# Optimization experiments

Measured on AMD Instinct MI355X. Metric: run time of the kernel, lower is better.

The kernel has to match this reference:

```python
import jax, jax.numpy as jnp
import numpy as np

B, CIN, COUT, T = 64, 2048, 2048, 128
BLOCK = 8            # structured-sparsity block size from _create_structured_sparse_mask
SPARSITY = 0.9       # keep probability per block = 1 - SPARSITY
SPIKE_PROB = 0.1     # binary input spike rate


def setup_inputs() -> dict:
    key = jax.random.key(0)
    k1, k2, k3 = jax.random.split(key, 3)
    # binary input spikes [B, Cin, T] (torch casts to int8; values are 0/1)
    spikes = (jax.random.uniform(k1, (B, CIN, T)) < SPIKE_PROB).astype(jnp.float32)
    # int8 quantized weights held as float32 (values in [-127,127))
    weights = jax.random.randint(k2, (COUT, CIN), -127, 127).astype(jnp.float32)
    # block-structured sparse connectivity mask, block 8x8, keep prob 0.1
    keep = jax.random.uniform(k3, (COUT // BLOCK, CIN // BLOCK)) > SPARSITY
    mask = jnp.repeat(jnp.repeat(keep, BLOCK, axis=0), BLOCK, axis=1).astype(jnp.float32)
    scale_exp = jnp.zeros((COUT,), dtype=jnp.int32)  # weight_scale_exp init zeros
    return {"spikes": spikes, "weights": weights, "mask": mask,
            "scale_exp": scale_exp, "threshold_exp": 7}


def reference(spikes, weights, mask, scale_exp, threshold_exp):
    # spikes: [B, Cin, T]; weights/mask: [Cout, Cin]; scale_exp: [Cout]
    masked_w = weights * mask                              # [Cout, Cin]
    scale = jnp.exp2(scale_exp.astype(jnp.float32))        # 2**weight_scale_exp per channel
    thr = jnp.float32(2.0) ** threshold_exp                # 2**threshold_exp (=128)
    s_t = jnp.transpose(spikes, (2, 0, 1))                 # [T, B, Cin]
    acc0 = jnp.zeros((spikes.shape[0], weights.shape[0]), jnp.float32)

    def step(acc, st):
        # integrate: sparse-masked matmul + power-of-two per-channel scale
        acc = acc + (st @ masked_w.T) * scale              # [B, Cout]
        spk = (acc >= thr).astype(jnp.float32)             # fire
        acc = acc * (1.0 - spk)                            # reset fired neurons to 0
        return acc, spk

    _, out = jax.lax.scan(step, acc0, s_t)                 # out: [T, B, Cout]
    return jnp.transpose(out, (1, 2, 0))                   # [B, Cout, T]
```

## Files before the change

kernel.cpp:

```cpp
#include <hip/hip_runtime.h>
#include <hip/hip_bf16.h>

#define BB   64
#define CIN  2048
#define COUT 2048
#define TT   128

typedef int i32x4 __attribute__((ext_vector_type(4)));

__device__ __forceinline__ void async16(char* lds_dst, const char* g_src) {
    __builtin_amdgcn_global_load_lds(
        (const __attribute__((address_space(1))) void*)g_src,
        (__attribute__((address_space(3))) void*)lds_dst,
        16, 0, 0);
}

__global__ void prep_kernel(const float* __restrict__ spikes,
                            const float* __restrict__ w,
                            const float* __restrict__ msk,
                            char* __restrict__ A,
                            char* __restrict__ Wm) {
    __shared__ float tile[64][33];
    int bid = blockIdx.x;
    int tid = threadIdx.x;

    if (bid < 1024) {
        size_t i = ((size_t)bid * 256 + tid) * 16;
        int out4[4];
#pragma unroll
        for (int q = 0; q < 4; ++q) {
            float4 a = *(const float4*)(w + i + q * 4);
            float4 m = *(const float4*)(msk + i + q * 4);
            int b0 = (int)(char)(int)(a.x * m.x);
            int b1 = (int)(char)(int)(a.y * m.y);
            int b2 = (int)(char)(int)(a.z * m.z);
            int b3 = (int)(char)(int)(a.w * m.w);
            out4[q] = (b0 & 0xFF) | ((b1 & 0xFF) << 8) | ((b2 & 0xFF) << 16) | (b3 << 24);
        }
        *(int4*)(Wm + i) = *(int4*)out4;
        return;
    }

    bid -= 1024;
    int cc = bid & 31;
    int tt = (bid >> 5) & 3;
    int b  = bid >> 7;
    int c0 = cc * 64, t0 = tt * 32;

    int t4 = tid & 7;
    int cr = tid >> 3;
#pragma unroll
    for (int s = 0; s < 2; ++s) {
        int c = cr + s * 32;
        float4 v = *(const float4*)(spikes + ((size_t)b * CIN + c0 + c) * TT + t0 + t4 * 4);
        tile[c][t4 * 4 + 0] = v.x;
        tile[c][t4 * 4 + 1] = v.y;
        tile[c][t4 * 4 + 2] = v.z;
        tile[c][t4 * 4 + 3] = v.w;
    }
    __syncthreads();

    int tw_ = tid >> 4;
    int cq  = tid & 15;
#pragma unroll
    for (int s2 = 0; s2 < 2; ++s2) {
        int tw = tw_ + s2 * 16;
        int packed = 0;
#pragma unroll
        for (int q = 0; q < 4; ++q)
            packed |= ((tile[cq * 4 + q][tw] != 0.f) ? 1 : 0) << (8 * q);
        *(int*)(A + ((size_t)(b * TT) + t0 + tw) * CIN + c0 + cq * 4) = packed;
    }
}

__global__ void __launch_bounds__(256, 4)
snn_gemm_scan(const char* __restrict__ A,
              const char* __restrict__ Wm,
              const int* __restrict__ scale_exp,
              const int* __restrict__ thr_exp,
              float* __restrict__ out) {
    __shared__ __align__(16) union {
        struct { char a[128 * 128]; char b[128 * 128]; } st;
        float c[128 * 68];
    } lds;
    __shared__ unsigned pb[64 * 4];

    const int tid  = threadIdx.x;
    const int lane = tid & 63;
    const int w    = tid >> 6;

    int flat = blockIdx.x;
    int xcd = flat & 7, idx = flat >> 3;
    int b  = xcd * 8 + (idx >> 4);
    int n0 = (idx & 15) * 128;
    int m0 = b * TT;

    int rr = tid >> 3;
    int cg = (tid & 7) ^ (rr & 7);
    const char* gAt = A  + (size_t)(m0 + rr) * CIN + cg * 16;
    const char* gBt = Wm + (size_t)(n0 + rr) * CIN + cg * 16;
    char* sA = (char*)lds.st.a;
    char* sB = (char*)lds.st.b;

    const int wm = (w >> 1) * 64, wn = (w & 1) * 64;
    const int mrow = lane & 15, kc = lane >> 4;
    unsigned offA[4], offB[4];
#pragma unroll
    for (int i = 0; i < 4; ++i) {
        offA[i] = (unsigned)(((wm + i * 16 + mrow) * 8 + (kc ^ (mrow & 7))) * 16);
        offB[i] = (unsigned)(((wn + i * 16 + mrow) * 8 + (kc ^ (mrow & 7))) * 16);
    }

    i32x4 acc[4][4] = {};
    for (int k0 = 0; k0 < CIN; k0 += 128) {
        __syncthreads();
#pragma unroll
        for (int i = 0; i < 4; ++i) {
            async16(sA + (unsigned)(tid + 256 * i) * 16, gAt + k0 + (size_t)(32 * i) * CIN);
            async16(sB + (unsigned)(tid + 256 * i) * 16, gBt + k0 + (size_t)(32 * i) * CIN);
        }
        __syncthreads();

#pragma unroll
        for (int s = 0; s < 2; ++s) {
            const unsigned sx = (unsigned)(s * 64);
            i32x4 av[4], bv[4];
#pragma unroll
            for (int i = 0; i < 4; ++i) av[i] = *(const i32x4*)(sA + (offA[i] ^ sx));
#pragma unroll
            for (int j = 0; j < 4; ++j) bv[j] = *(const i32x4*)(sB + (offB[j] ^ sx));
#pragma unroll
            for (int i = 0; i < 4; ++i)
#pragma unroll
                for (int j = 0; j < 4; ++j)
                    acc[i][j] = __builtin_amdgcn_mfma_i32_16x16x64_i8(
                        av[i], bv[j], acc[i][j], 0, 0, 0);
        }
    }

    const float thr = exp2f((float)thr_exp[0]);

#pragma unroll
    for (int p = 0; p < 2; ++p) {
        __syncthreads();
        if ((w & 1) == p) {
            const int rb = (lane >> 4) * 4;
            const int cb = lane & 15;
#pragma unroll
            for (int i = 0; i < 4; ++i)
#pragma unroll
                for (int j = 0; j < 4; ++j)
#pragma unroll
                    for (int r = 0; r < 4; ++r)
                        lds.c[(wm + i * 16 + rb + r) * 68 + (j * 16 + cb)] =
                            (float)acc[i][j][r];
        }
        __syncthreads();

        if (tid < 64) {
            float scale = exp2f((float)scale_exp[n0 + p * 64 + tid]);
            float a = 0.f;
            unsigned bits[4] = {0u, 0u, 0u, 0u};
#pragma unroll 4
            for (int t = 0; t < 128; ++t) {
                a += lds.c[t * 68 + tid] * scale;
                unsigned s = (a >= thr) ? 1u : 0u;
                if (s) a = 0.f;
                bits[t >> 5] |= s << (t & 31);
            }
#pragma unroll
            for (int q = 0; q < 4; ++q) pb[tid * 4 + q] = bits[q];
        }
        __syncthreads();

        const int t4 = tid & 31, cr = tid >> 5;
#pragma unroll
        for (int s2 = 0; s2 < 8; ++s2) {
            int co = s2 * 8 + cr;
            unsigned wb  = pb[co * 4 + (t4 >> 3)];
            unsigned nib = (wb >> ((t4 & 7) * 4)) & 0xFu;
            float4 v;
            v.x = (float)(nib & 1u);
            v.y = (float)((nib >> 1) & 1u);
            v.z = (float)((nib >> 2) & 1u);
            v.w = (float)((nib >> 3) & 1u);
            *(float4*)(out + (size_t)(b * COUT + n0 + p * 64 + co) * TT + t4 * 4) = v;
        }
    }
}

extern "C" void kernel_launch(void* const* d_in, const int* in_sizes, int n_in,
                              void* d_out, int out_size, void* d_ws, size_t ws_size,
                              hipStream_t stream) {
    const float* spikes  = (const float*)d_in[0];
    const float* weights = (const float*)d_in[1];
    const float* mask    = (const float*)d_in[2];
    const int*   scale_e = (const int*)d_in[3];
    const int*   thr_e   = (const int*)d_in[4];
    float* out = (float*)d_out;

    char* Ai8 = (char*)d_ws;
    char* Wm  = (char*)d_ws + (size_t)BB * TT * CIN;

    prep_kernel<<<1024 + BB * 4 * 32, 256, 0, stream>>>(spikes, weights, mask, Ai8, Wm);
    snn_gemm_scan<<<BB * (COUT / 128), 256, 0, stream>>>(Ai8, Wm, scale_e, thr_e, out);
}
```

Measured before the change: 183.5 us.

## Double-buffer K tiles with async LDS loads and rotate K start per block

```diff
diff --git a/kernel.cpp b/kernel.cpp
--- a/kernel.cpp
+++ b/kernel.cpp
@@ -80,7 +80,7 @@
               const int* __restrict__ thr_exp,
               float* __restrict__ out) {
     __shared__ __align__(16) union {
-        struct { char a[128 * 128]; char b[128 * 128]; } st;
+        struct { char a[2][128 * 64]; char b[2][128 * 64]; } st;
         float c[128 * 68];
     } lds;
     __shared__ unsigned pb[64 * 4];
@@ -95,10 +95,12 @@
     int n0 = (idx & 15) * 128;
     int m0 = b * TT;
 
-    int rr = tid >> 3;
-    int cg = (tid & 7) ^ (rr & 7);
-    const char* gAt = A  + (size_t)(m0 + rr) * CIN + cg * 16;
-    const char* gBt = Wm + (size_t)(n0 + rr) * CIN + cg * 16;
+    int rA = tid >> 2;
+    int cA = (tid & 3) ^ (rA & 3);
+    const char* gA0 = A  + (size_t)(m0 + rA) * CIN + cA * 16;
+    const char* gA1 = gA0 + (size_t)64 * CIN;
+    const char* gB0 = Wm + (size_t)(n0 + rA) * CIN + cA * 16;
+    const char* gB1 = gB0 + (size_t)64 * CIN;
     char* sA = (char*)lds.st.a;
     char* sB = (char*)lds.st.b;
 
@@ -107,35 +109,44 @@
     unsigned offA[4], offB[4];
 #pragma unroll
     for (int i = 0; i < 4; ++i) {
-        offA[i] = (unsigned)(((wm + i * 16 + mrow) * 8 + (kc ^ (mrow & 7))) * 16);
-        offB[i] = (unsigned)(((wn + i * 16 + mrow) * 8 + (kc ^ (mrow & 7))) * 16);
+        offA[i] = (unsigned)(((wm + i * 16 + mrow) * 4 + (kc ^ (mrow & 3))) * 16);
+        offB[i] = (unsigned)(((wn + i * 16 + mrow) * 4 + (kc ^ (mrow & 3))) * 16);
+    }
+
+    const int krot = flat & 31;
+
+    {
+        int k = ((krot) & 31) << 6;
+        async16(sA + tid * 16,         gA0 + k);
+        async16(sA + (tid + 256) * 16, gA1 + k);
+        async16(sB + tid * 16,         gB0 + k);
+        async16(sB + (tid + 256) * 16, gB1 + k);
     }
 
     i32x4 acc[4][4] = {};
-    for (int k0 = 0; k0 < CIN; k0 += 128) {
-        __syncthreads();
-#pragma unroll
-        for (int i = 0; i < 4; ++i) {
-            async16(sA + (unsigned)(tid + 256 * i) * 16, gAt + k0 + (size_t)(32 * i) * CIN);
-            async16(sB + (unsigned)(tid + 256 * i) * 16, gBt + k0 + (size_t)(32 * i) * CIN);
-        }
-        __syncthreads();
-
-#pragma unroll
-        for (int s = 0; s < 2; ++s) {
-            const unsigned sx = (unsigned)(s * 64);
-            i32x4 av[4], bv[4];
-#pragma unroll
-            for (int i = 0; i < 4; ++i) av[i] = *(const i32x4*)(sA + (offA[i] ^ sx));
-#pragma unroll
-            for (int j = 0; j < 4; ++j) bv[j] = *(const i32x4*)(sB + (offB[j] ^ sx));
-#pragma unroll
-            for (int i = 0; i < 4; ++i)
-#pragma unroll
-                for (int j = 0; j < 4; ++j)
-                    acc[i][j] = __builtin_amdgcn_mfma_i32_16x16x64_i8(
-                        av[i], bv[j], acc[i][j], 0, 0, 0);
-        }
+    for (int i = 0; i < 32; ++i) {
+        __syncthreads();
+        if (i < 31) {
+            int k = ((i + 1 + krot) & 31) << 6;
+            unsigned nb = (unsigned)(((i + 1) & 1) * 8192);
+            async16(sA + nb + tid * 16,         gA0 + k);
+            async16(sA + nb + (tid + 256) * 16, gA1 + k);
+            async16(sB + nb + tid * 16,         gB0 + k);
+            async16(sB + nb + (tid + 256) * 16, gB1 + k);
+        }
+        const char* bufA = sA + (unsigned)((i & 1) * 8192);
+        const char* bufB = sB + (unsigned)((i & 1) * 8192);
+        i32x4 av[4], bv[4];
+#pragma unroll
+        for (int ii = 0; ii < 4; ++ii) av[ii] = *(const i32x4*)(bufA + offA[ii]);
+#pragma unroll
+        for (int jj = 0; jj < 4; ++jj) bv[jj] = *(const i32x4*)(bufB + offB[jj]);
+#pragma unroll
+        for (int ii = 0; ii < 4; ++ii)
+#pragma unroll
+            for (int jj = 0; jj < 4; ++jj)
+                acc[ii][jj] = __builtin_amdgcn_mfma_i32_16x16x64_i8(
+                    av[ii], bv[jj], acc[ii][jj], 0, 0, 0);
     }
 
     const float thr = exp2f((float)thr_exp[0]);
```

New measurement: 188.5 us. +2.7%, slower.

## Double-buffer LDS tiles to overlap global loads with MFMA compute

Applied to the files above, without the earlier changes.

```diff
diff --git a/kernel.cpp b/kernel.cpp
--- a/kernel.cpp
+++ b/kernel.cpp
@@ -73,14 +73,14 @@
     }
 }
 
-__global__ void __launch_bounds__(256, 4)
+__global__ void __launch_bounds__(256, 2)
 snn_gemm_scan(const char* __restrict__ A,
               const char* __restrict__ Wm,
               const int* __restrict__ scale_exp,
               const int* __restrict__ thr_exp,
               float* __restrict__ out) {
     __shared__ __align__(16) union {
-        struct { char a[128 * 128]; char b[128 * 128]; } st;
+        struct { char a[2][128 * 128]; char b[2][128 * 128]; } st;
         float c[128 * 68];
     } lds;
     __shared__ unsigned pb[64 * 4];
@@ -99,8 +99,6 @@
     int cg = (tid & 7) ^ (rr & 7);
     const char* gAt = A  + (size_t)(m0 + rr) * CIN + cg * 16;
     const char* gBt = Wm + (size_t)(n0 + rr) * CIN + cg * 16;
-    char* sA = (char*)lds.st.a;
-    char* sB = (char*)lds.st.b;
 
     const int wm = (w >> 1) * 64, wn = (w & 1) * 64;
     const int mrow = lane & 15, kc = lane >> 4;
@@ -111,30 +109,47 @@
         offB[i] = (unsigned)(((wn + i * 16 + mrow) * 8 + (kc ^ (mrow & 7))) * 16);
     }
 
+#pragma unroll
+    for (int q = 0; q < 4; ++q) {
+        async16((char*)lds.st.a[0] + (unsigned)(tid + 256 * q) * 16,
+                gAt + (size_t)(32 * q) * CIN);
+        async16((char*)lds.st.b[0] + (unsigned)(tid + 256 * q) * 16,
+                gBt + (size_t)(32 * q) * CIN);
+    }
+
     i32x4 acc[4][4] = {};
-    for (int k0 = 0; k0 < CIN; k0 += 128) {
-        __syncthreads();
-#pragma unroll
-        for (int i = 0; i < 4; ++i) {
-            async16(sA + (unsigned)(tid + 256 * i) * 16, gAt + k0 + (size_t)(32 * i) * CIN);
-            async16(sB + (unsigned)(tid + 256 * i) * 16, gBt + k0 + (size_t)(32 * i) * CIN);
-        }
-        __syncthreads();
-
+    for (int it = 0; it < 16; ++it) {
+        asm volatile("s_waitcnt vmcnt(0)\n\ts_barrier" ::: "memory");
+
+        if (it < 15) {
+            int k = (it + 1) * 128;
+            char* nA = (char*)lds.st.a[(it + 1) & 1];
+            char* nB = (char*)lds.st.b[(it + 1) & 1];
+#pragma unroll
+            for (int q = 0; q < 4; ++q) {
+                async16(nA + (unsigned)(tid + 256 * q) * 16,
+                        gAt + k + (size_t)(32 * q) * CIN);
+                async16(nB + (unsigned)(tid + 256 * q) * 16,
+                        gBt + k + (size_t)(32 * q) * CIN);
+            }
+        }
+
+        const char* bufA = (const char*)lds.st.a[it & 1];
+        const char* bufB = (const char*)lds.st.b[it & 1];
 #pragma unroll
         for (int s = 0; s < 2; ++s) {
             const unsigned sx = (unsigned)(s * 64);
             i32x4 av[4], bv[4];
 #pragma unroll
-            for (int i = 0; i < 4; ++i) av[i] = *(const i32x4*)(sA + (offA[i] ^ sx));
-#pragma unroll
-            for (int j = 0; j < 4; ++j) bv[j] = *(const i32x4*)(sB + (offB[j] ^ sx));
-#pragma unroll
-            for (int i = 0; i < 4; ++i)
-#pragma unroll
-                for (int j = 0; j < 4; ++j)
-                    acc[i][j] = __builtin_amdgcn_mfma_i32_16x16x64_i8(
-                        av[i], bv[j], acc[i][j], 0, 0, 0);
+            for (int ii = 0; ii < 4; ++ii) av[ii] = *(const i32x4*)(bufA + (offA[ii] ^ sx));
+#pragma unroll
+            for (int jj = 0; jj < 4; ++jj) bv[jj] = *(const i32x4*)(bufB + (offB[jj] ^ sx));
+#pragma unroll
+            for (int ii = 0; ii < 4; ++ii)
+#pragma unroll
+                for (int jj = 0; jj < 4; ++jj)
+                    acc[ii][jj] = __builtin_amdgcn_mfma_i32_16x16x64_i8(
+                        av[ii], bv[jj], acc[ii][jj], 0, 0, 0);
         }
     }
 
```

Measured after the change: 199.4 us. +8.6%, slower.

## Exploit block-sparse mask with compacted weight blocks and gathered int8 MFMA

Applied to the files above, without the earlier changes.

```diff
diff --git a/kernel.cpp b/kernel.cpp
--- a/kernel.cpp
+++ b/kernel.cpp
@@ -1,191 +1,183 @@
 #include <hip/hip_runtime.h>
-#include <hip/hip_bf16.h>
 
 #define BB   64
 #define CIN  2048
 #define COUT 2048
 #define TT   128
+#define NG   128
+#define NCB  256
+#define CAPC 24
 
 typedef int i32x4 __attribute__((ext_vector_type(4)));
 
-__device__ __forceinline__ void async16(char* lds_dst, const char* g_src) {
-    __builtin_amdgcn_global_load_lds(
-        (const __attribute__((address_space(1))) void*)g_src,
-        (__attribute__((address_space(3))) void*)lds_dst,
-        16, 0, 0);
-}
+#define OFF_WC   16777216ull
+#define OFF_GIDX 19922944ull
+#define OFF_GCNT 19972096ull
 
 __global__ void prep_kernel(const float* __restrict__ spikes,
-                            const float* __restrict__ w,
-                            const float* __restrict__ msk,
-                            char* __restrict__ A,
-                            char* __restrict__ Wm) {
-    __shared__ float tile[64][33];
-    int bid = blockIdx.x;
-    int tid = threadIdx.x;
-
-    if (bid < 1024) {
-        size_t i = ((size_t)bid * 256 + tid) * 16;
-        int out4[4];
-#pragma unroll
-        for (int q = 0; q < 4; ++q) {
-            float4 a = *(const float4*)(w + i + q * 4);
-            float4 m = *(const float4*)(msk + i + q * 4);
-            int b0 = (int)(char)(int)(a.x * m.x);
-            int b1 = (int)(char)(int)(a.y * m.y);
-            int b2 = (int)(char)(int)(a.z * m.z);
-            int b3 = (int)(char)(int)(a.w * m.w);
-            out4[q] = (b0 & 0xFF) | ((b1 & 0xFF) << 8) | ((b2 & 0xFF) << 16) | (b3 << 24);
+                            const float* __restrict__ weights,
+                            const float* __restrict__ mask,
+                            char* __restrict__ A_blk,
+                            char* __restrict__ Wc,
+                            unsigned short* __restrict__ gidx,
+                            int* __restrict__ gcnt) {
+    __shared__ union {
+        float tile[64][33];
+        struct { unsigned short sidx[CAPC * 8]; int wcnt[4]; } c;
+    } sm;
+    int bid = blockIdx.x, tid = threadIdx.x;
+
+    if (bid < NG) {
+        int g = bid;
+        int lane = tid & 63, wv = tid >> 6;
+        int j = tid;
+        bool nz = (mask[(size_t)(16 * g) * CIN + 8 * j] != 0.f) ||
+                  (mask[(size_t)(16 * g + 8) * CIN + 8 * j] != 0.f);
+        unsigned long long bal = __ballot(nz);
+        if (lane == 0) sm.c.wcnt[wv] = (int)__popcll(bal);
+        __syncthreads();
+        int cnt = sm.c.wcnt[0] + sm.c.wcnt[1] + sm.c.wcnt[2] + sm.c.wcnt[3];
+        int pre = 0;
+#pragma unroll
+        for (int ww = 0; ww < 4; ++ww) if (ww < wv) pre += sm.c.wcnt[ww];
+        int rank = pre + (int)__popcll(bal & ((1ull << lane) - 1ull));
+        int nk = (cnt + 7) >> 3; if (nk > CAPC) nk = CAPC;
+        int ns = nk * 8;
+        if (nz && rank < ns) sm.c.sidx[rank] = (unsigned short)j;
+        if (tid >= cnt && tid < ns) sm.c.sidx[tid] = 0;
+        if (tid == 0) gcnt[g] = nk;
+        __syncthreads();
+        if (tid < ns) gidx[g * (CAPC * 8) + tid] = sm.c.sidx[tid];
+
+        for (int base = 0; base < ns; base += 16) {
+            int s = base + (tid >> 4);
+            if (s < ns) {
+                int n = tid & 15;
+                int js = sm.c.sidx[s];
+                bool live = (s < cnt) &&
+                            (mask[(size_t)(16 * g + n) * CIN + js * 8] != 0.f);
+                const float* wr = weights + (size_t)(16 * g + n) * CIN + js * 8;
+                float4 w0 = *(const float4*)wr;
+                float4 w1 = *(const float4*)(wr + 4);
+                unsigned lo = 0, hi = 0;
+                if (live) {
+                    lo = ((unsigned)((char)(int)w0.x) & 0xFF)
+                       | ((((unsigned)((char)(int)w0.y)) & 0xFF) << 8)
+                       | ((((unsigned)((char)(int)w0.z)) & 0xFF) << 16)
+                       | (((unsigned)((char)(int)w0.w)) << 24);
+                    hi = ((unsigned)((char)(int)w1.x) & 0xFF)
+                       | ((((unsigned)((char)(int)w1.y)) & 0xFF) << 8)
+                       | ((((unsigned)((char)(int)w1.z)) & 0xFF) << 16)
+                       | (((unsigned)((char)(int)w1.w)) << 24);
+                }
+                int2 pv; pv.x = (int)lo; pv.y = (int)hi;
+                *(int2*)(Wc + ((size_t)(g * CAPC + (s >> 3)) * 16 + n) * 64 +
+                         (s & 7) * 8) = pv;
+            }
         }
-        *(int4*)(Wm + i) = *(int4*)out4;
         return;
     }
 
-    bid -= 1024;
+    bid -= NG;
     int cc = bid & 31;
     int tt = (bid >> 5) & 3;
     int b  = bid >> 7;
     int c0 = cc * 64, t0 = tt * 32;
 
-    int t4 = tid & 7;
-    int cr = tid >> 3;
+    int t4 = tid & 7, cr = tid >> 3;
 #pragma unroll
     for (int s = 0; s < 2; ++s) {
         int c = cr + s * 32;
         float4 v = *(const float4*)(spikes + ((size_t)b * CIN + c0 + c) * TT + t0 + t4 * 4);
-        tile[c][t4 * 4 + 0] = v.x;
-        tile[c][t4 * 4 + 1] = v.y;
-        tile[c][t4 * 4 + 2] = v.z;
-        tile[c][t4 * 4 + 3] = v.w;
+        sm.tile[c][t4 * 4 + 0] = v.x;
+        sm.tile[c][t4 * 4 + 1] = v.y;
+        sm.tile[c][t4 * 4 + 2] = v.z;
+        sm.tile[c][t4 * 4 + 3] = v.w;
     }
     __syncthreads();
 
-    int tw_ = tid >> 4;
-    int cq  = tid & 15;
-#pragma unroll
-    for (int s2 = 0; s2 < 2; ++s2) {
-        int tw = tw_ + s2 * 16;
-        int packed = 0;
-#pragma unroll
-        for (int q = 0; q < 4; ++q)
-            packed |= ((tile[cq * 4 + q][tw] != 0.f) ? 1 : 0) << (8 * q);
-        *(int*)(A + ((size_t)(b * TT) + t0 + tw) * CIN + c0 + cq * 4) = packed;
-    }
+    int cb_l = tid >> 5;
+    int t_l  = tid & 31;
+    unsigned lo = 0, hi = 0;
+#pragma unroll
+    for (int jj = 0; jj < 4; ++jj)
+        lo |= (sm.tile[cb_l * 8 + jj][t_l] != 0.f ? 1u : 0u) << (8 * jj);
+#pragma unroll
+    for (int jj = 0; jj < 4; ++jj)
+        hi |= (sm.tile[cb_l * 8 + 4 + jj][t_l] != 0.f ? 1u : 0u) << (8 * jj);
+    int2 pv; pv.x = (int)lo; pv.y = (int)hi;
+    *(int2*)(A_blk + ((size_t)((b * NCB + cc * 8 + cb_l) * TT) + t0 + t_l) * 8) = pv;
 }
 
 __global__ void __launch_bounds__(256, 4)
-snn_gemm_scan(const char* __restrict__ A,
-              const char* __restrict__ Wm,
-              const int* __restrict__ scale_exp,
-              const int* __restrict__ thr_exp,
-              float* __restrict__ out) {
-    __shared__ __align__(16) union {
-        struct { char a[128 * 128]; char b[128 * 128]; } st;
-        float c[128 * 68];
-    } lds;
-    __shared__ unsigned pb[64 * 4];
-
-    const int tid  = threadIdx.x;
-    const int lane = tid & 63;
-    const int w    = tid >> 6;
-
-    int flat = blockIdx.x;
-    int xcd = flat & 7, idx = flat >> 3;
-    int b  = xcd * 8 + (idx >> 4);
-    int n0 = (idx & 15) * 128;
-    int m0 = b * TT;
-
-    int rr = tid >> 3;
-    int cg = (tid & 7) ^ (rr & 7);
-    const char* gAt = A  + (size_t)(m0 + rr) * CIN + cg * 16;
-    const char* gBt = Wm + (size_t)(n0 + rr) * CIN + cg * 16;
-    char* sA = (char*)lds.st.a;
-    char* sB = (char*)lds.st.b;
-
-    const int wm = (w >> 1) * 64, wn = (w & 1) * 64;
-    const int mrow = lane & 15, kc = lane >> 4;
-    unsigned offA[4], offB[4];
-#pragma unroll
-    for (int i = 0; i < 4; ++i) {
-        offA[i] = (unsigned)(((wm + i * 16 + mrow) * 8 + (kc ^ (mrow & 7))) * 16);
-        offB[i] = (unsigned)(((wn + i * 16 + mrow) * 8 + (kc ^ (mrow & 7))) * 16);
-    }
-
-    i32x4 acc[4][4] = {};
-    for (int k0 = 0; k0 < CIN; k0 += 128) {
-        __syncthreads();
-#pragma unroll
-        for (int i = 0; i < 4; ++i) {
-            async16(sA + (unsigned)(tid + 256 * i) * 16, gAt + k0 + (size_t)(32 * i) * CIN);
-            async16(sB + (unsigned)(tid + 256 * i) * 16, gBt + k0 + (size_t)(32 * i) * CIN);
+snn_sparse(const char* __restrict__ A_blk,
+           const char* __restrict__ Wc,
+           const unsigned short* __restrict__ gidx,
+           const int* __restrict__ gcnt,
+           const int* __restrict__ scale_exp,
+           const int* __restrict__ thr_exp,
+           float* __restrict__ out) {
+    __shared__ float ldsC[4][TT * 18];
+
+    const int tid = threadIdx.x, lane = tid & 63, wv = tid >> 6;
+    const int bid = blockIdx.x;
+    const int b = bid >> 5, q = bid & 31;
+    const int g = q * 4 + wv;
+
+    const int nk = gcnt[g];
+    const unsigned short* idx = gidx + g * (CAPC * 8);
+    const char* wcg = Wc + (size_t)g * CAPC * 1024;
+    const char* ab  = A_blk + (size_t)b * (NCB * TT * 8);
+
+    const int m  = lane & 15;
+    const int kq = lane >> 4;
+
+    i32x4 acc[8] = {};
+    for (int ck = 0; ck < nk; ++ck) {
+        unsigned pair = *(const unsigned*)(idx + ck * 8 + kq * 2);
+        unsigned s0 = pair & 0xFFFFu, s1 = pair >> 16;
+        i32x4 bfrag = *(const i32x4*)(wcg + ck * 1024 + m * 64 + kq * 16);
+        const char* a0p = ab + ((size_t)s0 << 10) + m * 8;
+        const char* a1p = ab + ((size_t)s1 << 10) + m * 8;
+#pragma unroll
+        for (int mt = 0; mt < 8; ++mt) {
+            int2 a0 = *(const int2*)(a0p + mt * 128);
+            int2 a1 = *(const int2*)(a1p + mt * 128);
+            i32x4 af; af[0] = a0.x; af[1] = a0.y; af[2] = a1.x; af[3] = a1.y;
+            acc[mt] = __builtin_amdgcn_mfma_i32_16x16x64_i8(af, bfrag, acc[mt], 0, 0, 0);
         }
-        __syncthreads();
-
-#pragma unroll
-        for (int s = 0; s < 2; ++s) {
-            const unsigned sx = (unsigned)(s * 64);
-            i32x4 av[4], bv[4];
-#pragma unroll
-            for (int i = 0; i < 4; ++i) av[i] = *(const i32x4*)(sA + (offA[i] ^ sx));
-#pragma unroll
-            for (int j = 0; j < 4; ++j) bv[j] = *(const i32x4*)(sB + (offB[j] ^ sx));
-#pragma unroll
-            for (int i = 0; i < 4; ++i)
-#pragma unroll
-                for (int j = 0; j < 4; ++j)
-                    acc[i][j] = __builtin_amdgcn_mfma_i32_16x16x64_i8(
-                        av[i], bv[j], acc[i][j], 0, 0, 0);
-        }
-    }
-
-    const float thr = exp2f((float)thr_exp[0]);
-
-#pragma unroll
-    for (int p = 0; p < 2; ++p) {
-        __syncthreads();
-        if ((w & 1) == p) {
-            const int rb = (lane >> 4) * 4;
-            const int cb = lane & 15;
-#pragma unroll
-            for (int i = 0; i < 4; ++i)
-#pragma unroll
-                for (int j = 0; j < 4; ++j)
-#pragma unroll
-                    for (int r = 0; r < 4; ++r)
-                        lds.c[(wm + i * 16 + rb + r) * 68 + (j * 16 + cb)] =
-                            (float)acc[i][j][r];
-        }
-        __syncthreads();
-
-        if (tid < 64) {
-            float scale = exp2f((float)scale_exp[n0 + p * 64 + tid]);
-            float a = 0.f;
-            unsigned bits[4] = {0u, 0u, 0u, 0u};
+    }
+
+    float* lc = ldsC[wv];
+#pragma unroll
+    for (int mt = 0; mt < 8; ++mt)
+#pragma unroll
+        for (int r = 0; r < 4; ++r)
+            lc[(mt * 16 + kq * 4 + r) * 18 + m] = (float)acc[mt][r];
+
+    const float scale = exp2f((float)scale_exp[g * 16 + m]);
+    const float thr   = exp2f((float)thr_exp[0]);
+    float a = 0.f;
+    unsigned bits[4] = {0u, 0u, 0u, 0u};
 #pragma unroll 4
-            for (int t = 0; t < 128; ++t) {
-                a += lds.c[t * 68 + tid] * scale;
-                unsigned s = (a >= thr) ? 1u : 0u;
-                if (s) a = 0.f;
-                bits[t >> 5] |= s << (t & 31);
-            }
-#pragma unroll
-            for (int q = 0; q < 4; ++q) pb[tid * 4 + q] = bits[q];
-        }
-        __syncthreads();
-
-        const int t4 = tid & 31, cr = tid >> 5;
-#pragma unroll
-        for (int s2 = 0; s2 < 8; ++s2) {
-            int co = s2 * 8 + cr;
-            unsigned wb  = pb[co * 4 + (t4 >> 3)];
-            unsigned nib = (wb >> ((t4 & 7) * 4)) & 0xFu;
-            float4 v;
-            v.x = (float)(nib & 1u);
-            v.y = (float)((nib >> 1) & 1u);
-            v.z = (float)((nib >> 2) & 1u);
-            v.w = (float)((nib >> 3) & 1u);
-            *(float4*)(out + (size_t)(b * COUT + n0 + p * 64 + co) * TT + t4 * 4) = v;
-        }
+    for (int t = 0; t < TT; ++t) {
+        a += lc[t * 18 + m] * scale;
+        unsigned s = (a >= thr) ? 1u : 0u;
+        if (s) a = 0.f;
+        bits[t >> 5] |= s << (t & 31);
+    }
+
+    unsigned wb = bits[kq];
+    float* op = out + ((size_t)(b * COUT + g * 16 + m)) * TT + kq * 32;
+#pragma unroll
+    for (int s2 = 0; s2 < 8; ++s2) {
+        unsigned nib = (wb >> (s2 * 4)) & 0xFu;
+        float4 v;
+        v.x = (float)(nib & 1u);
+        v.y = (float)((nib >> 1) & 1u);
+        v.z = (float)((nib >> 2) & 1u);
+        v.w = (float)((nib >> 3) & 1u);
+        *(float4*)(op + s2 * 4) = v;
     }
 }
 
@@ -199,9 +191,13 @@
     const int*   thr_e   = (const int*)d_in[4];
     float* out = (float*)d_out;
 
-    char* Ai8 = (char*)d_ws;
-    char* Wm  = (char*)d_ws + (size_t)BB * TT * CIN;
-
-    prep_kernel<<<1024 + BB * 4 * 32, 256, 0, stream>>>(spikes, weights, mask, Ai8, Wm);
-    snn_gemm_scan<<<BB * (COUT / 128), 256, 0, stream>>>(Ai8, Wm, scale_e, thr_e, out);
+    char* A_blk = (char*)d_ws;
+    char* Wc    = (char*)d_ws + OFF_WC;
+    unsigned short* gidx = (unsigned short*)((char*)d_ws + OFF_GIDX);
+    int* gcnt = (int*)((char*)d_ws + OFF_GCNT);
+
+    prep_kernel<<<NG + BB * 4 * 32, 256, 0, stream>>>(spikes, weights, mask,
+                                                      A_blk, Wc, gidx, gcnt);
+    snn_sparse<<<BB * 32, 256, 0, stream>>>(A_blk, Wc, gidx, gcnt,
+                                            scale_e, thr_e, out);
 }
```

Result: slower. 190.2 us (+3.7%).
